# Optimization experiments

Hardware: AMD Instinct MI355X
Metric: run time of the kernel (lower is better)

Reference implementation:

```python
import jax, jax.numpy as jnp
import numpy as np

V, D, K = 50000, 300, 50      # vocab, embed_dim, dim_latent (topics)
B, S, N, L = 32, 8192, 128, 64  # batch, doc len, segments/doc, max seg len (=stride)


def setup_inputs() -> dict:
    key = jax.random.key(0)
    k0, k1, k2, k3, k4, k5 = jax.random.split(key, 6)
    embedding = jax.random.normal(k0, (V, D), jnp.float32) * 0.02
    M_w = jax.random.normal(k1, (D, D), jnp.float32) / np.sqrt(D).astype(np.float32)
    W_w = jax.random.normal(k2, (K, D), jnp.float32) / np.sqrt(D).astype(np.float32)
    T_w = jax.random.normal(k3, (D, K), jnp.float32) / np.sqrt(K).astype(np.float32)
    input_tensor = jax.random.randint(k4, (B, S), 0, V)
    # non-overlapping segments with stride L; ragged lengths in [8, L]
    seg_starts = jnp.broadcast_to(jnp.arange(N, dtype=jnp.int32) * L, (B, N))
    seg_lens = jax.random.randint(k5, (B, N), 8, L + 1)
    return {"embedding": embedding, "M_w": M_w, "W_w": W_w, "T_w": T_w,
            "input_tensor": input_tensor, "seg_starts": seg_starts, "seg_lens": seg_lens}


def reference(embedding, M_w, W_w, T_w, input_tensor, seg_starts, seg_lens):
    # Build padded segment token grid + mask (vectorized version of the
    # per-batch Python loop in the original forward).
    offs = jnp.arange(L)
    pos = seg_starts[..., None] + offs                       # [B,N,L]
    mask = (offs < seg_lens[..., None]).astype(embedding.dtype)  # [B,N,L]
    tok = jnp.take_along_axis(input_tensor, pos.reshape(B, N * L), axis=1).reshape(B, N, L)
    sub_emb = embedding[tok] * mask[..., None]               # [B,N,L,D] (zeros at pad)
    # masked mean over segment tokens
    y = sub_emb.sum(axis=2) / jnp.maximum(mask.sum(axis=2), 1.0)[..., None]  # [B,N,D]
    # attention score: (M @ e_l) . y, masked softmax
    esc = jnp.einsum('bnld,ed,bne->bnl', sub_emb, M_w, y)    # M(x) = x @ M_w.T
    esc = jnp.where(mask > 0, esc, -1e9)
    alpha = jax.nn.softmax(esc, axis=-1)                     # [B,N,L]
    z = jnp.einsum('bnl,bnld->bnd', alpha, sub_emb)          # [B,N,D]
    p = jax.nn.softmax(z @ W_w.T, axis=-1)                   # [B,N,K]
    r = p @ T_w.T                                            # [B,N,D]
    return y, z, p, r
```

## Files before the change

### kernel.cpp

```cpp
#include <hip/hip_runtime.h>
#include <hip/hip_fp16.h>

#define DD 300
#define KK 50
#define BB 32
#define SS 8192
#define NN 128
#define LL 64
#define NSEG (BB * NN)
#define NW 5
#define NT 320
#define NJ 13
#define TM 8

__device__ __forceinline__ float wave_sum(float v) {
    #pragma unroll
    for (int m = 32; m; m >>= 1) v += __shfl_xor(v, m, 64);
    return v;
}
__device__ __forceinline__ float wave_max(float v) {
    #pragma unroll
    for (int m = 32; m; m >>= 1) v = fmaxf(v, __shfl_xor(v, m, 64));
    return v;
}
__device__ __forceinline__ unsigned int pack_h2(float a, float b) {
    __half2 h = __floats2half2_rn(a, b);
    return *reinterpret_cast<const unsigned int*>(&h);
}
__device__ __forceinline__ float2 unpack_h2(unsigned int v) {
    __half2 h = *reinterpret_cast<const __half2*>(&v);
    return __half22float2(h);
}

__global__ __launch_bounds__(NT) void k_y(
    const float* __restrict__ emb,
    const int*   __restrict__ tokens,
    const int*   __restrict__ seg_starts,
    const int*   __restrict__ seg_lens,
    float* __restrict__ out_y)
{
    __shared__ int    tok_s[LL];
    __shared__ float4 part4[NW][75];

    const int tid  = threadIdx.x;
    const int wave = tid >> 6;
    const int lane = tid & 63;
    const int seg  = blockIdx.x;
    const int b    = seg >> 7;
    const int start = seg_starts[seg];
    const int len   = seg_lens[seg];

    if (tid < LL) tok_s[tid] = tokens[b * SS + start + tid];
    __syncthreads();

    float4 a0 = {0.f, 0.f, 0.f, 0.f};
    float4 a1 = {0.f, 0.f, 0.f, 0.f};
    #pragma unroll
    for (int j = 0; j < NJ; ++j) {
        const int l  = wave + j * NW;
        const int lc = (l < len) ? l : (len - 1);
        const float4* row4 = (const float4*)(emb + (size_t)tok_s[lc] * DD);
        const float4 r0 = row4[lane];
        float4 r1 = {0.f, 0.f, 0.f, 0.f};
        if (lane < 11) r1 = row4[64 + lane];
        const float m = (l < len) ? 1.f : 0.f;
        a0.x += m * r0.x; a0.y += m * r0.y; a0.z += m * r0.z; a0.w += m * r0.w;
        a1.x += m * r1.x; a1.y += m * r1.y; a1.z += m * r1.z; a1.w += m * r1.w;
    }
    part4[wave][lane] = a0;
    if (lane < 11) part4[wave][64 + lane] = a1;
    __syncthreads();

    if (tid < 75) {
        float4 s = {0.f, 0.f, 0.f, 0.f};
        #pragma unroll
        for (int w = 0; w < NW; ++w) {
            const float4 pv = part4[w][tid];
            s.x += pv.x; s.y += pv.y; s.z += pv.z; s.w += pv.w;
        }
        const float inv = 1.f / (float)len;
        s.x *= inv; s.y *= inv; s.z *= inv; s.w *= inv;
        ((float4*)(out_y + (size_t)seg * DD))[tid] = s;
    }
}

__global__ __launch_bounds__(NT) void k_u(
    const float* __restrict__ y,
    const float* __restrict__ M_w,
    float* __restrict__ u)
{
    const int tid  = threadIdx.x;
    const int row0 = blockIdx.x * TM;
    if (tid >= DD) return;

    float acc[TM];
    #pragma unroll
    for (int r = 0; r < TM; ++r) acc[r] = 0.f;

    #pragma unroll 5
    for (int e = 0; e < DD; ++e) {
        const float m = M_w[(size_t)e * DD + tid];
        #pragma unroll
        for (int r = 0; r < TM; ++r)
            acc[r] += m * y[(size_t)(row0 + r) * DD + e];
    }
    #pragma unroll
    for (int r = 0; r < TM; ++r)
        u[(size_t)(row0 + r) * DD + tid] = acc[r];
}

__global__ __launch_bounds__(NT) void k_rest(
    const float* __restrict__ emb,
    const float* __restrict__ W_w,
    const float* __restrict__ T_w,
    const int*   __restrict__ tokens,
    const int*   __restrict__ seg_starts,
    const int*   __restrict__ seg_lens,
    const float* __restrict__ u_ws,
    float* __restrict__ out_z,
    float* __restrict__ out_p,
    float* __restrict__ out_r)
{
    __shared__ int    tok_s[LL];
    __shared__ uint2  e_s[LL][75];
    __shared__ float  a_s[LL + 1];
    __shared__ float2 zp_s[NW][150];
    __shared__ float  z_s[NT];
    __shared__ float  p_s[64];

    const int tid  = threadIdx.x;
    const int wave = tid >> 6;
    const int lane = tid & 63;
    const int seg  = blockIdx.x;
    const int b    = seg >> 7;
    const int start = seg_starts[seg];
    const int len   = seg_lens[seg];

    if (tid < LL) tok_s[tid] = tokens[b * SS + start + tid];
    __syncthreads();

    float4 u0, u1 = {0.f, 0.f, 0.f, 0.f};
    {
        const float4* up4 = (const float4*)(u_ws + (size_t)seg * DD);
        u0 = up4[lane];
        if (lane < 11) u1 = up4[64 + lane];
    }

    #pragma unroll
    for (int j = 0; j < NJ; ++j) {
        const int l  = wave + j * NW;
        const int lc = (l < len) ? l : (len - 1);
        const float4* row4 = (const float4*)(emb + (size_t)tok_s[lc] * DD);
        const float4 r0 = row4[lane];
        float4 r1 = {0.f, 0.f, 0.f, 0.f};
        if (lane < 11) r1 = row4[64 + lane];

        if (l < LL) {
            e_s[l][lane] = make_uint2(pack_h2(r0.x, r0.y), pack_h2(r0.z, r0.w));
            if (lane < 11)
                e_s[l][64 + lane] = make_uint2(pack_h2(r1.x, r1.y), pack_h2(r1.z, r1.w));
        }

        float dot = r0.x * u0.x + r0.y * u0.y + r0.z * u0.z + r0.w * u0.w
                  + r1.x * u1.x + r1.y * u1.y + r1.z * u1.z + r1.w * u1.w;
        dot = wave_sum(dot);
        if (lane == 0 && l < len) a_s[l] = dot;
    }
    if (tid == NT - 1) a_s[LL] = 0.f;
    __syncthreads();

    if (wave == 0) {
        const float v  = (lane < len) ? a_s[lane] : -INFINITY;
        const float mx = wave_max(v);
        const float e  = (lane < len) ? __expf(v - mx) : 0.f;
        const float sm = wave_sum(e);
        a_s[lane] = e / sm;
    }
    __syncthreads();

    {
        float2 zA = {0.f, 0.f}, zB = {0.f, 0.f}, zC = {0.f, 0.f};
        #pragma unroll
        for (int j = 0; j < NJ; ++j) {
            const int l  = wave + j * NW;
            const int lr = (l < LL) ? l : (LL - 1);
            const float a = a_s[l];
            const unsigned int* ru = (const unsigned int*)&e_s[lr][0];
            const float2 fA = unpack_h2(ru[lane]);
            const float2 fB = unpack_h2(ru[64 + lane]);
            zA.x += a * fA.x; zA.y += a * fA.y;
            zB.x += a * fB.x; zB.y += a * fB.y;
            if (lane < 22) {
                const float2 fC = unpack_h2(ru[128 + lane]);
                zC.x += a * fC.x; zC.y += a * fC.y;
            }
        }
        zp_s[wave][lane]      = zA;
        zp_s[wave][64 + lane] = zB;
        if (lane < 22) zp_s[wave][128 + lane] = zC;
    }
    __syncthreads();

    if (tid < 150) {
        float2 s = {0.f, 0.f};
        #pragma unroll
        for (int w = 0; w < NW; ++w) {
            const float2 pv = zp_s[w][tid];
            s.x += pv.x; s.y += pv.y;
        }
        z_s[2 * tid]     = s.x;
        z_s[2 * tid + 1] = s.y;
        ((float2*)(out_z + (size_t)seg * DD))[tid] = s;
    }
    __syncthreads();

    for (int k = wave; k < KK; k += NW) {
        const float* wr = W_w + (size_t)k * DD;
        float d0 = wr[lane] * z_s[lane] + wr[lane + 64] * z_s[lane + 64]
                 + wr[lane + 128] * z_s[lane + 128] + wr[lane + 192] * z_s[lane + 192];
        if (lane < 44) d0 += wr[lane + 256] * z_s[lane + 256];
        d0 = wave_sum(d0);
        if (lane == 0) p_s[k] = d0;
    }
    __syncthreads();

    if (wave == 0) {
        const float v  = (lane < KK) ? p_s[lane] : -INFINITY;
        const float mx = wave_max(v);
        const float e  = (lane < KK) ? __expf(v - mx) : 0.f;
        const float sm = wave_sum(e);
        if (lane < KK) {
            const float p = e / sm;
            p_s[lane] = p;
            out_p[(size_t)seg * KK + lane] = p;
        }
    }
    __syncthreads();

    if (tid < DD) {
        const float* trow = T_w + (size_t)tid * KK;
        float acc = 0.f;
        #pragma unroll
        for (int k = 0; k < KK; ++k) acc += p_s[k] * trow[k];
        out_r[(size_t)seg * DD + tid] = acc;
    }
}

extern "C" void kernel_launch(void* const* d_in, const int* in_sizes, int n_in,
                              void* d_out, int out_size, void* d_ws, size_t ws_size,
                              hipStream_t stream) {
    const float* emb        = (const float*)d_in[0];
    const float* M_w        = (const float*)d_in[1];
    const float* W_w        = (const float*)d_in[2];
    const float* T_w        = (const float*)d_in[3];
    const int*   tokens     = (const int*)d_in[4];
    const int*   seg_starts = (const int*)d_in[5];
    const int*   seg_lens   = (const int*)d_in[6];

    float* out   = (float*)d_out;
    float* out_y = out;
    float* out_z = out + (size_t)NSEG * DD;
    float* out_p = out + (size_t)2 * NSEG * DD;
    float* out_r = out + (size_t)2 * NSEG * DD + (size_t)NSEG * KK;

    float* u_ws = (float*)d_ws;

    hipLaunchKernelGGL(k_y, dim3(NSEG), dim3(NT), 0, stream,
                       emb, tokens, seg_starts, seg_lens, out_y);
    hipLaunchKernelGGL(k_u, dim3(NSEG / TM), dim3(NT), 0, stream,
                       out_y, M_w, u_ws);
    hipLaunchKernelGGL(k_rest, dim3(NSEG), dim3(NT), 0, stream,
                       emb, W_w, T_w, tokens, seg_starts, seg_lens,
                       u_ws, out_z, out_p, out_r);
}
```

Measured before the change: 224.4 us.

## Batch embedding gathers and compute attention scores from padded LDS rows

Both gather kernels now issue seven row loads per batch before consuming any of them, with a schedule barrier in between, so more memory requests are in flight at once. The divergent 11-lane tail load is replaced by a second overlapping full-wave load at offset 11. In k_rest the per-row wave_sum score reduction is dropped: embeddings go into a padded fp16 LDS buffer (row stride 151 to avoid bank conflicts), and each lane then computes a partial dot product for one token over a 60-element slice of D, with the five wave partials summed before the softmax. The overlapping loads and stores add redundant memory traffic, and the batched loads raise register pressure.

```diff
diff --git a/kernel.cpp b/kernel.cpp
--- a/kernel.cpp
+++ b/kernel.cpp
@@ -12,6 +12,7 @@
 #define NT 320
 #define NJ 13
 #define TM 8
+#define RS 151
 
 __device__ __forceinline__ float wave_sum(float v) {
     #pragma unroll
@@ -53,22 +54,34 @@
     if (tid < LL) tok_s[tid] = tokens[b * SS + start + tid];
     __syncthreads();
 
-    float4 a0 = {0.f, 0.f, 0.f, 0.f};
-    float4 a1 = {0.f, 0.f, 0.f, 0.f};
-    #pragma unroll
-    for (int j = 0; j < NJ; ++j) {
-        const int l  = wave + j * NW;
-        const int lc = (l < len) ? l : (len - 1);
-        const float4* row4 = (const float4*)(emb + (size_t)tok_s[lc] * DD);
-        const float4 r0 = row4[lane];
-        float4 r1 = {0.f, 0.f, 0.f, 0.f};
-        if (lane < 11) r1 = row4[64 + lane];
-        const float m = (l < len) ? 1.f : 0.f;
-        a0.x += m * r0.x; a0.y += m * r0.y; a0.z += m * r0.z; a0.w += m * r0.w;
-        a1.x += m * r1.x; a1.y += m * r1.y; a1.z += m * r1.z; a1.w += m * r1.w;
-    }
-    part4[wave][lane] = a0;
-    if (lane < 11) part4[wave][64 + lane] = a1;
+    float4 accA = {0.f, 0.f, 0.f, 0.f};
+    float4 accB = {0.f, 0.f, 0.f, 0.f};
+    #pragma unroll
+    for (int jb = 0; jb < 2; ++jb) {
+        const int j0 = jb * 7;
+        const int j1 = (jb == 0) ? 7 : NJ;
+        float4 A[7], B[7];
+        #pragma unroll
+        for (int j = j0; j < j1; ++j) {
+            const int l  = wave + j * NW;
+            const int lc = (l < len) ? l : (len - 1);
+            const float4* row4 = (const float4*)(emb + (size_t)tok_s[lc] * DD);
+            A[j - j0] = row4[lane];
+            B[j - j0] = row4[11 + lane];
+        }
+        __builtin_amdgcn_sched_barrier(0);
+        #pragma unroll
+        for (int j = j0; j < j1; ++j) {
+            const int l = wave + j * NW;
+            const float m = (l < len) ? 1.f : 0.f;
+            accA.x += m * A[j - j0].x; accA.y += m * A[j - j0].y;
+            accA.z += m * A[j - j0].z; accA.w += m * A[j - j0].w;
+            accB.x += m * B[j - j0].x; accB.y += m * B[j - j0].y;
+            accB.z += m * B[j - j0].z; accB.w += m * B[j - j0].w;
+        }
+    }
+    part4[wave][lane]      = accA;
+    part4[wave][11 + lane] = accB;
     __syncthreads();
 
     if (tid < 75) {
@@ -121,8 +134,10 @@
     float* __restrict__ out_p,
     float* __restrict__ out_r)
 {
+    __shared__ unsigned int e16[LL * RS];
     __shared__ int    tok_s[LL];
-    __shared__ uint2  e_s[LL][75];
+    __shared__ float  u_s[304];
+    __shared__ float  pe_s[NW][LL];
     __shared__ float  a_s[LL + 1];
     __shared__ float2 zp_s[NW][150];
     __shared__ float  z_s[NT];
@@ -137,40 +152,55 @@
     const int len   = seg_lens[seg];
 
     if (tid < LL) tok_s[tid] = tokens[b * SS + start + tid];
-    __syncthreads();
-
-    float4 u0, u1 = {0.f, 0.f, 0.f, 0.f};
+    if (tid < 75) ((float4*)u_s)[tid] = ((const float4*)(u_ws + (size_t)seg * DD))[tid];
+    __syncthreads();
+
+    #pragma unroll
+    for (int jb = 0; jb < 2; ++jb) {
+        const int j0 = jb * 7;
+        const int j1 = (jb == 0) ? 7 : NJ;
+        float4 A[7], B[7];
+        #pragma unroll
+        for (int j = j0; j < j1; ++j) {
+            const int l  = wave + j * NW;
+            const int lc = (l < len) ? l : (len - 1);
+            const float4* row4 = (const float4*)(emb + (size_t)tok_s[lc] * DD);
+            A[j - j0] = row4[lane];
+            B[j - j0] = row4[11 + lane];
+        }
+        __builtin_amdgcn_sched_barrier(0);
+        #pragma unroll
+        for (int j = j0; j < j1; ++j) {
+            const int l = wave + j * NW;
+            if (l < LL) {
+                unsigned int* rw = &e16[l * RS];
+                rw[2 * lane]      = pack_h2(A[j - j0].x, A[j - j0].y);
+                rw[2 * lane + 1]  = pack_h2(A[j - j0].z, A[j - j0].w);
+                rw[22 + 2 * lane] = pack_h2(B[j - j0].x, B[j - j0].y);
+                rw[23 + 2 * lane] = pack_h2(B[j - j0].z, B[j - j0].w);
+            }
+        }
+    }
+    __syncthreads();
+
     {
-        const float4* up4 = (const float4*)(u_ws + (size_t)seg * DD);
-        u0 = up4[lane];
-        if (lane < 11) u1 = up4[64 + lane];
-    }
-
-    #pragma unroll
-    for (int j = 0; j < NJ; ++j) {
-        const int l  = wave + j * NW;
-        const int lc = (l < len) ? l : (len - 1);
-        const float4* row4 = (const float4*)(emb + (size_t)tok_s[lc] * DD);
-        const float4 r0 = row4[lane];
-        float4 r1 = {0.f, 0.f, 0.f, 0.f};
-        if (lane < 11) r1 = row4[64 + lane];
-
-        if (l < LL) {
-            e_s[l][lane] = make_uint2(pack_h2(r0.x, r0.y), pack_h2(r0.z, r0.w));
-            if (lane < 11)
-                e_s[l][64 + lane] = make_uint2(pack_h2(r1.x, r1.y), pack_h2(r1.z, r1.w));
-        }
-
-        float dot = r0.x * u0.x + r0.y * u0.y + r0.z * u0.z + r0.w * u0.w
-                  + r1.x * u1.x + r1.y * u1.y + r1.z * u1.z + r1.w * u1.w;
-        dot = wave_sum(dot);
-        if (lane == 0 && l < len) a_s[l] = dot;
+        const int c0 = 30 * wave;
+        const unsigned int* myrow = &e16[lane * RS];
+        float acc = 0.f;
+        #pragma unroll
+        for (int c = 0; c < 30; ++c) {
+            const float2 ef = unpack_h2(myrow[c0 + c]);
+            acc += ef.x * u_s[2 * (c0 + c)] + ef.y * u_s[2 * (c0 + c) + 1];
+        }
+        pe_s[wave][lane] = acc;
     }
     if (tid == NT - 1) a_s[LL] = 0.f;
     __syncthreads();
 
     if (wave == 0) {
-        const float v  = (lane < len) ? a_s[lane] : -INFINITY;
+        const float esc = pe_s[0][lane] + pe_s[1][lane] + pe_s[2][lane]
+                        + pe_s[3][lane] + pe_s[4][lane];
+        const float v  = (lane < len) ? esc : -INFINITY;
         const float mx = wave_max(v);
         const float e  = (lane < len) ? __expf(v - mx) : 0.f;
         const float sm = wave_sum(e);
@@ -185,7 +215,7 @@
             const int l  = wave + j * NW;
             const int lr = (l < LL) ? l : (LL - 1);
             const float a = a_s[l];
-            const unsigned int* ru = (const unsigned int*)&e_s[lr][0];
+            const unsigned int* ru = &e16[lr * RS];
             const float2 fA = unpack_h2(ru[lane]);
             const float2 fB = unpack_h2(ru[64 + lane]);
             zA.x += a * fA.x; zA.y += a * fA.y;
```

Result: faster. 186.5 us (-16.9%).

## Fuse mean and M-projection kernels, process multiple segments per block with prefetch

Applied to the files above, without the earlier changes.

Merges the y-mean kernel and the u = M·y projection into one kernel that handles four segments per block, so the y round-trip through global memory and one launch go away. Both remaining kernels now loop over four segments each and issue the embedding-row loads for the next segment while computing the current one, using register double-buffering and sched barriers. Row loads switch to overlapping float4 reads (lanes 0-63 and 11-74) to drop the divergent tail load, and the shared-memory row stride is padded. Trade-offs are higher register pressure from the 26 float4 prefetch registers, a quarter as many blocks, and raw s_barrier/waitcnt sync that depends on the exact lgkm ordering.

```diff
diff --git a/kernel.cpp b/kernel.cpp
--- a/kernel.cpp
+++ b/kernel.cpp
@@ -11,7 +11,9 @@
 #define NW 5
 #define NT 320
 #define NJ 13
-#define TM 8
+#define GY 4
+#define GR 4
+#define RSU 152
 
 __device__ __forceinline__ float wave_sum(float v) {
     #pragma unroll
@@ -32,84 +34,109 @@
     return __half22float2(h);
 }
 
-__global__ __launch_bounds__(NT) void k_y(
+__device__ __forceinline__ void issue_rows(const float* __restrict__ emb,
+    int tok, int len, int wave, int lane, float4* A, float4* B)
+{
+    #pragma unroll
+    for (int j = 0; j < NJ; ++j) {
+        const int l  = wave + j * NW;
+        const int lc = (l < len) ? l : (len - 1);
+        const int t  = __shfl(tok, lc);
+        const float4* row4 = (const float4*)(emb + (size_t)t * DD);
+        A[j] = row4[lane];
+        B[j] = row4[11 + lane];
+    }
+    __builtin_amdgcn_sched_barrier(0);
+}
+
+__global__ __launch_bounds__(NT, 3) void k_yu(
     const float* __restrict__ emb,
+    const float* __restrict__ M_w,
     const int*   __restrict__ tokens,
     const int*   __restrict__ seg_starts,
     const int*   __restrict__ seg_lens,
-    float* __restrict__ out_y)
+    float* __restrict__ out_y,
+    float* __restrict__ u_ws)
 {
-    __shared__ int    tok_s[LL];
-    __shared__ float4 part4[NW][75];
+    __shared__ float4 part4[GY][NW][75];
+    __shared__ float4 y4_s[GY][75];
 
     const int tid  = threadIdx.x;
     const int wave = tid >> 6;
     const int lane = tid & 63;
-    const int seg  = blockIdx.x;
-    const int b    = seg >> 7;
-    const int start = seg_starts[seg];
-    const int len   = seg_lens[seg];
-
-    if (tid < LL) tok_s[tid] = tokens[b * SS + start + tid];
+    const int seg0 = blockIdx.x * GY;
+
+    int lens[GY], bases[GY];
+    #pragma unroll
+    for (int s = 0; s < GY; ++s) {
+        const int seg = seg0 + s;
+        lens[s]  = seg_lens[seg];
+        bases[s] = (seg >> 7) * SS + seg_starts[seg];
+    }
+
+    float4 A[NJ], B[NJ];
+    const int tokc = tokens[bases[0] + lane];
+    issue_rows(emb, tokc, lens[0], wave, lane, A, B);
+
+    #pragma unroll
+    for (int s = 0; s < GY; ++s) {
+        int tokn = 0;
+        if (s + 1 < GY) tokn = tokens[bases[s + 1] + lane];
+        float4 aA = make_float4(0.f, 0.f, 0.f, 0.f);
+        float4 aB = make_float4(0.f, 0.f, 0.f, 0.f);
+        #pragma unroll
+        for (int j = 0; j < NJ; ++j) {
+            const int l = wave + j * NW;
+            const float m = (l < lens[s]) ? 1.f : 0.f;
+            aA.x += m * A[j].x; aA.y += m * A[j].y; aA.z += m * A[j].z; aA.w += m * A[j].w;
+            aB.x += m * B[j].x; aB.y += m * B[j].y; aB.z += m * B[j].z; aB.w += m * B[j].w;
+        }
+        if (s + 1 < GY) issue_rows(emb, tokn, lens[s + 1], wave, lane, A, B);
+        part4[s][wave][lane]      = aA;
+        part4[s][wave][11 + lane] = aB;
+    }
     __syncthreads();
 
-    float4 a0 = {0.f, 0.f, 0.f, 0.f};
-    float4 a1 = {0.f, 0.f, 0.f, 0.f};
-    #pragma unroll
-    for (int j = 0; j < NJ; ++j) {
-        const int l  = wave + j * NW;
-        const int lc = (l < len) ? l : (len - 1);
-        const float4* row4 = (const float4*)(emb + (size_t)tok_s[lc] * DD);
-        const float4 r0 = row4[lane];
-        float4 r1 = {0.f, 0.f, 0.f, 0.f};
-        if (lane < 11) r1 = row4[64 + lane];
-        const float m = (l < len) ? 1.f : 0.f;
-        a0.x += m * r0.x; a0.y += m * r0.y; a0.z += m * r0.z; a0.w += m * r0.w;
-        a1.x += m * r1.x; a1.y += m * r1.y; a1.z += m * r1.z; a1.w += m * r1.w;
-    }
-    part4[wave][lane] = a0;
-    if (lane < 11) part4[wave][64 + lane] = a1;
-    __syncthreads();
-
-    if (tid < 75) {
-        float4 s = {0.f, 0.f, 0.f, 0.f};
+    if (tid < 300) {
+        const int s = tid / 75, c = tid - s * 75;
+        float4 sum = make_float4(0.f, 0.f, 0.f, 0.f);
         #pragma unroll
         for (int w = 0; w < NW; ++w) {
-            const float4 pv = part4[w][tid];
-            s.x += pv.x; s.y += pv.y; s.z += pv.z; s.w += pv.w;
-        }
-        const float inv = 1.f / (float)len;
-        s.x *= inv; s.y *= inv; s.z *= inv; s.w *= inv;
-        ((float4*)(out_y + (size_t)seg * DD))[tid] = s;
-    }
-}
-
-__global__ __launch_bounds__(NT) void k_u(
-    const float* __restrict__ y,
-    const float* __restrict__ M_w,
-    float* __restrict__ u)
-{
-    const int tid  = threadIdx.x;
-    const int row0 = blockIdx.x * TM;
-    if (tid >= DD) return;
-
-    float acc[TM];
-    #pragma unroll
-    for (int r = 0; r < TM; ++r) acc[r] = 0.f;
-
-    #pragma unroll 5
-    for (int e = 0; e < DD; ++e) {
-        const float m = M_w[(size_t)e * DD + tid];
-        #pragma unroll
-        for (int r = 0; r < TM; ++r)
-            acc[r] += m * y[(size_t)(row0 + r) * DD + e];
-    }
-    #pragma unroll
-    for (int r = 0; r < TM; ++r)
-        u[(size_t)(row0 + r) * DD + tid] = acc[r];
-}
-
-__global__ __launch_bounds__(NT) void k_rest(
+            const float4 pv = part4[s][w][c];
+            sum.x += pv.x; sum.y += pv.y; sum.z += pv.z; sum.w += pv.w;
+        }
+        const float inv = 1.f / (float)seg_lens[seg0 + s];
+        sum.x *= inv; sum.y *= inv; sum.z *= inv; sum.w *= inv;
+        y4_s[s][c] = sum;
+        ((float4*)(out_y + (size_t)(seg0 + s) * DD))[c] = sum;
+    }
+    __syncthreads();
+
+    if (tid < DD) {
+        float acc0 = 0.f, acc1 = 0.f, acc2 = 0.f, acc3 = 0.f;
+        #pragma unroll 3
+        for (int e4 = 0; e4 < 75; ++e4) {
+            const float m0 = M_w[(size_t)(4 * e4 + 0) * DD + tid];
+            const float m1 = M_w[(size_t)(4 * e4 + 1) * DD + tid];
+            const float m2 = M_w[(size_t)(4 * e4 + 2) * DD + tid];
+            const float m3 = M_w[(size_t)(4 * e4 + 3) * DD + tid];
+            const float4 y0 = y4_s[0][e4];
+            const float4 y1 = y4_s[1][e4];
+            const float4 y2 = y4_s[2][e4];
+            const float4 y3 = y4_s[3][e4];
+            acc0 += m0 * y0.x + m1 * y0.y + m2 * y0.z + m3 * y0.w;
+            acc1 += m0 * y1.x + m1 * y1.y + m2 * y1.z + m3 * y1.w;
+            acc2 += m0 * y2.x + m1 * y2.y + m2 * y2.z + m3 * y2.w;
+            acc3 += m0 * y3.x + m1 * y3.y + m2 * y3.z + m3 * y3.w;
+        }
+        u_ws[(size_t)(seg0 + 0) * DD + tid] = acc0;
+        u_ws[(size_t)(seg0 + 1) * DD + tid] = acc1;
+        u_ws[(size_t)(seg0 + 2) * DD + tid] = acc2;
+        u_ws[(size_t)(seg0 + 3) * DD + tid] = acc3;
+    }
+}
+
+__global__ __launch_bounds__(NT, 3) void k_rest(
     const float* __restrict__ emb,
     const float* __restrict__ W_w,
     const float* __restrict__ T_w,
@@ -121,128 +148,143 @@
     float* __restrict__ out_p,
     float* __restrict__ out_r)
 {
-    __shared__ int    tok_s[LL];
-    __shared__ uint2  e_s[LL][75];
+    __shared__ unsigned int e16[LL * RSU];
     __shared__ float  a_s[LL + 1];
-    __shared__ float2 zp_s[NW][150];
-    __shared__ float  z_s[NT];
+    __shared__ float2 zp_s[NW][152];
+    __shared__ float  z_s[304];
     __shared__ float  p_s[64];
 
     const int tid  = threadIdx.x;
     const int wave = tid >> 6;
     const int lane = tid & 63;
-    const int seg  = blockIdx.x;
-    const int b    = seg >> 7;
-    const int start = seg_starts[seg];
-    const int len   = seg_lens[seg];
-
-    if (tid < LL) tok_s[tid] = tokens[b * SS + start + tid];
-    __syncthreads();
-
-    float4 u0, u1 = {0.f, 0.f, 0.f, 0.f};
+    const int seg0 = blockIdx.x * GR;
+
+    int lens[GR], bases[GR];
+    #pragma unroll
+    for (int s = 0; s < GR; ++s) {
+        const int seg = seg0 + s;
+        lens[s]  = seg_lens[seg];
+        bases[s] = (seg >> 7) * SS + seg_starts[seg];
+    }
+    if (tid == 0) a_s[LL] = 0.f;
+
+    float4 A[NJ], B[NJ];
+    float4 U0, U1;
+    const int tokc = tokens[bases[0] + lane];
+    issue_rows(emb, tokc, lens[0], wave, lane, A, B);
     {
-        const float4* up4 = (const float4*)(u_ws + (size_t)seg * DD);
-        u0 = up4[lane];
-        if (lane < 11) u1 = up4[64 + lane];
-    }
-
-    #pragma unroll
-    for (int j = 0; j < NJ; ++j) {
-        const int l  = wave + j * NW;
-        const int lc = (l < len) ? l : (len - 1);
-        const float4* row4 = (const float4*)(emb + (size_t)tok_s[lc] * DD);
-        const float4 r0 = row4[lane];
-        float4 r1 = {0.f, 0.f, 0.f, 0.f};
-        if (lane < 11) r1 = row4[64 + lane];
-
-        if (l < LL) {
-            e_s[l][lane] = make_uint2(pack_h2(r0.x, r0.y), pack_h2(r0.z, r0.w));
-            if (lane < 11)
-                e_s[l][64 + lane] = make_uint2(pack_h2(r1.x, r1.y), pack_h2(r1.z, r1.w));
-        }
-
-        float dot = r0.x * u0.x + r0.y * u0.y + r0.z * u0.z + r0.w * u0.w
-                  + r1.x * u1.x + r1.y * u1.y + r1.z * u1.z + r1.w * u1.w;
-        dot = wave_sum(dot);
-        if (lane == 0 && l < len) a_s[l] = dot;
-    }
-    if (tid == NT - 1) a_s[LL] = 0.f;
-    __syncthreads();
-
-    if (wave == 0) {
-        const float v  = (lane < len) ? a_s[lane] : -INFINITY;
-        const float mx = wave_max(v);
-        const float e  = (lane < len) ? __expf(v - mx) : 0.f;
-        const float sm = wave_sum(e);
-        a_s[lane] = e / sm;
-    }
-    __syncthreads();
-
-    {
-        float2 zA = {0.f, 0.f}, zB = {0.f, 0.f}, zC = {0.f, 0.f};
+        const float4* up = (const float4*)(u_ws + (size_t)seg0 * DD);
+        U0 = up[lane];
+        const float4 u1r = up[11 + lane];
+        U1 = (lane >= 53) ? u1r : make_float4(0.f, 0.f, 0.f, 0.f);
+    }
+
+    #pragma unroll
+    for (int g = 0; g < GR; ++g) {
+        int tokn = 0;
+        if (g + 1 < GR) tokn = tokens[bases[g + 1] + lane];
         #pragma unroll
         for (int j = 0; j < NJ; ++j) {
-            const int l  = wave + j * NW;
-            const int lr = (l < LL) ? l : (LL - 1);
-            const float a = a_s[l];
-            const unsigned int* ru = (const unsigned int*)&e_s[lr][0];
-            const float2 fA = unpack_h2(ru[lane]);
-            const float2 fB = unpack_h2(ru[64 + lane]);
-            zA.x += a * fA.x; zA.y += a * fA.y;
-            zB.x += a * fB.x; zB.y += a * fB.y;
-            if (lane < 22) {
-                const float2 fC = unpack_h2(ru[128 + lane]);
-                zC.x += a * fC.x; zC.y += a * fC.y;
+            const int l = wave + j * NW;
+            float dot = A[j].x * U0.x + A[j].y * U0.y + A[j].z * U0.z + A[j].w * U0.w
+                      + B[j].x * U1.x + B[j].y * U1.y + B[j].z * U1.z + B[j].w * U1.w;
+            dot = wave_sum(dot);
+            if (lane == 0 && l < lens[g]) a_s[l] = dot;
+            if (l < LL) {
+                unsigned int* rw = &e16[l * RSU];
+                *(uint2*)&rw[2 * lane]      = make_uint2(pack_h2(A[j].x, A[j].y), pack_h2(A[j].z, A[j].w));
+                *(uint2*)&rw[22 + 2 * lane] = make_uint2(pack_h2(B[j].x, B[j].y), pack_h2(B[j].z, B[j].w));
             }
         }
-        zp_s[wave][lane]      = zA;
-        zp_s[wave][64 + lane] = zB;
-        if (lane < 22) zp_s[wave][128 + lane] = zC;
-    }
-    __syncthreads();
-
-    if (tid < 150) {
-        float2 s = {0.f, 0.f};
-        #pragma unroll
-        for (int w = 0; w < NW; ++w) {
-            const float2 pv = zp_s[w][tid];
-            s.x += pv.x; s.y += pv.y;
-        }
-        z_s[2 * tid]     = s.x;
-        z_s[2 * tid + 1] = s.y;
-        ((float2*)(out_z + (size_t)seg * DD))[tid] = s;
-    }
-    __syncthreads();
-
-    for (int k = wave; k < KK; k += NW) {
-        const float* wr = W_w + (size_t)k * DD;
-        float d0 = wr[lane] * z_s[lane] + wr[lane + 64] * z_s[lane + 64]
-                 + wr[lane + 128] * z_s[lane + 128] + wr[lane + 192] * z_s[lane + 192];
-        if (lane < 44) d0 += wr[lane + 256] * z_s[lane + 256];
-        d0 = wave_sum(d0);
-        if (lane == 0) p_s[k] = d0;
-    }
-    __syncthreads();
-
-    if (wave == 0) {
-        const float v  = (lane < KK) ? p_s[lane] : -INFINITY;
-        const float mx = wave_max(v);
-        const float e  = (lane < KK) ? __expf(v - mx) : 0.f;
-        const float sm = wave_sum(e);
-        if (lane < KK) {
-            const float p = e / sm;
-            p_s[lane] = p;
-            out_p[(size_t)seg * KK + lane] = p;
-        }
-    }
-    __syncthreads();
-
-    if (tid < DD) {
-        const float* trow = T_w + (size_t)tid * KK;
-        float acc = 0.f;
-        #pragma unroll
-        for (int k = 0; k < KK; ++k) acc += p_s[k] * trow[k];
-        out_r[(size_t)seg * DD + tid] = acc;
+        if (g + 1 < GR) {
+            issue_rows(emb, tokn, lens[g + 1], wave, lane, A, B);
+            const float4* up = (const float4*)(u_ws + (size_t)(seg0 + g + 1) * DD);
+            U0 = up[lane];
+            const float4 u1r = up[11 + lane];
+            U1 = (lane >= 53) ? u1r : make_float4(0.f, 0.f, 0.f, 0.f);
+            __builtin_amdgcn_sched_barrier(0);
+        }
+        asm volatile("s_waitcnt lgkmcnt(0)" ::: "memory");
+        __builtin_amdgcn_s_barrier();
+
+        if (wave == 0) {
+            const float v  = (lane < lens[g]) ? a_s[lane] : -INFINITY;
+            const float mx = wave_max(v);
+            const float e  = (lane < lens[g]) ? __expf(v - mx) : 0.f;
+            const float sm = wave_sum(e);
+            a_s[lane] = e / sm;
+        }
+        asm volatile("s_waitcnt lgkmcnt(0)" ::: "memory");
+        __builtin_amdgcn_s_barrier();
+
+        {
+            float2 zA = make_float2(0.f, 0.f), zB = make_float2(0.f, 0.f), zC = make_float2(0.f, 0.f);
+            #pragma unroll
+            for (int j = 0; j < NJ; ++j) {
+                const int l  = wave + j * NW;
+                const int lr = (l < LL) ? l : (LL - 1);
+                const float a = a_s[l];
+                const unsigned int* ru = &e16[lr * RSU];
+                const float2 fA = unpack_h2(ru[lane]);
+                const float2 fB = unpack_h2(ru[64 + lane]);
+                zA.x += a * fA.x; zA.y += a * fA.y;
+                zB.x += a * fB.x; zB.y += a * fB.y;
+                if (lane < 22) {
+                    const float2 fC = unpack_h2(ru[128 + lane]);
+                    zC.x += a * fC.x; zC.y += a * fC.y;
+                }
+            }
+            zp_s[wave][lane]      = zA;
+            zp_s[wave][64 + lane] = zB;
+            if (lane < 22) zp_s[wave][128 + lane] = zC;
+        }
+        asm volatile("s_waitcnt lgkmcnt(0)" ::: "memory");
+        __builtin_amdgcn_s_barrier();
+
+        if (tid < 150) {
+            float2 s = make_float2(0.f, 0.f);
+            #pragma unroll
+            for (int w = 0; w < NW; ++w) { const float2 pv = zp_s[w][tid]; s.x += pv.x; s.y += pv.y; }
+            z_s[2 * tid]     = s.x;
+            z_s[2 * tid + 1] = s.y;
+            ((float2*)(out_z + (size_t)(seg0 + g) * DD))[tid] = s;
+        }
+        asm volatile("s_waitcnt lgkmcnt(0)" ::: "memory");
+        __builtin_amdgcn_s_barrier();
+
+        for (int k = wave; k < KK; k += NW) {
+            const float* wr = W_w + (size_t)k * DD;
+            float d0 = wr[lane] * z_s[lane] + wr[lane + 64] * z_s[lane + 64]
+                     + wr[lane + 128] * z_s[lane + 128] + wr[lane + 192] * z_s[lane + 192];
+            if (lane < 44) d0 += wr[lane + 256] * z_s[lane + 256];
+            d0 = wave_sum(d0);
+            if (lane == 0) p_s[k] = d0;
+        }
+        asm volatile("s_waitcnt lgkmcnt(0)" ::: "memory");
+        __builtin_amdgcn_s_barrier();
+
+        if (wave == 0) {
+            const float v  = (lane < KK) ? p_s[lane] : -INFINITY;
+            const float mx = wave_max(v);
+            const float e  = (lane < KK) ? __expf(v - mx) : 0.f;
+            const float sm = wave_sum(e);
+            if (lane < KK) {
+                const float p = e / sm;
+                p_s[lane] = p;
+                out_p[(size_t)(seg0 + g) * KK + lane] = p;
+            }
+        }
+        asm volatile("s_waitcnt lgkmcnt(0)" ::: "memory");
+        __builtin_amdgcn_s_barrier();
+
+        if (tid < DD) {
+            const float* trow = T_w + (size_t)tid * KK;
+            float acc = 0.f;
+            #pragma unroll
+            for (int k = 0; k < KK; ++k) acc += p_s[k] * trow[k];
+            out_r[(size_t)(seg0 + g) * DD + tid] = acc;
+        }
+        __builtin_amdgcn_s_barrier();
     }
 }
 
@@ -265,11 +307,9 @@
 
     float* u_ws = (float*)d_ws;
 
-    hipLaunchKernelGGL(k_y, dim3(NSEG), dim3(NT), 0, stream,
-                       emb, tokens, seg_starts, seg_lens, out_y);
-    hipLaunchKernelGGL(k_u, dim3(NSEG / TM), dim3(NT), 0, stream,
-                       out_y, M_w, u_ws);
-    hipLaunchKernelGGL(k_rest, dim3(NSEG), dim3(NT), 0, stream,
+    hipLaunchKernelGGL(k_yu, dim3(NSEG / GY), dim3(NT), 0, stream,
+                       emb, M_w, tokens, seg_starts, seg_lens, out_y, u_ws);
+    hipLaunchKernelGGL(k_rest, dim3(NSEG / GR), dim3(NT), 0, stream,
                        emb, W_w, T_w, tokens, seg_starts, seg_lens,
                        u_ws, out_z, out_p, out_r);
 }
```

Measured after the change: 399.8 us. 78.2% more time.
